# Kernel optimization log

Hardware: AMD Instinct MI355X
Metric: run time of the kernel (lower is better)

The kernel has to match this reference:

```python
import jax, jax.numpy as jnp
import numpy as np
import math

N_HEADS = 16
D_KV = 64
D_MODEL = 1024
NUM_BUCKETS = 32
MAX_DISTANCE = 128


def _relative_position_bucket(rel_pos):
    # encoder (is_decoder=False): bidirectional buckets
    num_buckets = NUM_BUCKETS // 2  # 16
    rel_buckets = (rel_pos > 0).astype(jnp.int32) * num_buckets
    rel_pos = jnp.abs(rel_pos)
    max_exact = num_buckets // 2  # 8
    is_small = rel_pos < max_exact
    rel_pos_large = max_exact + (
        jnp.log(rel_pos.astype(jnp.float32) / max_exact)
        / math.log(MAX_DISTANCE / max_exact)
        * (num_buckets - max_exact)
    ).astype(jnp.int32)
    rel_pos_large = jnp.minimum(rel_pos_large, num_buckets - 1)
    return rel_buckets + jnp.where(is_small, rel_pos, rel_pos_large)


def setup_inputs() -> dict:
    key = jax.random.key(0)
    ks = jax.random.split(key, 6)
    s = 1.0 / math.sqrt(D_MODEL)
    return {
        "hidden_states": jax.random.normal(ks[0], (2, 2048, D_MODEL), jnp.float32),
        "Wq": jax.random.normal(ks[1], (D_MODEL, N_HEADS * D_KV), jnp.float32) * s,
        "Wk": jax.random.normal(ks[2], (D_MODEL, N_HEADS * D_KV), jnp.float32) * s,
        "Wv": jax.random.normal(ks[3], (D_MODEL, N_HEADS * D_KV), jnp.float32) * s,
        "Wo": jax.random.normal(ks[4], (N_HEADS * D_KV, D_MODEL), jnp.float32) * s,
        "rel_bias": jax.random.normal(ks[5], (NUM_BUCKETS, N_HEADS), jnp.float32),
    }


def reference(hidden_states, Wq, Wk, Wv, Wo, rel_bias):
    b, seq, _ = hidden_states.shape
    q = (hidden_states @ Wq).reshape(b, seq, N_HEADS, D_KV)
    k = (hidden_states @ Wk).reshape(b, seq, N_HEADS, D_KV)
    v = (hidden_states @ Wv).reshape(b, seq, N_HEADS, D_KV)

    # relative position bias: [1, n_heads, q_len, k_len]
    ctx = jnp.arange(seq, dtype=jnp.int32)[:, None]
    mem = jnp.arange(seq, dtype=jnp.int32)[None, :]
    buckets = _relative_position_bucket(mem - ctx)  # [q, k]
    pos_bias = rel_bias[buckets]                    # [q, k, h]
    pos_bias = jnp.transpose(pos_bias, (2, 0, 1))[None]  # [1, h, q, k]

    # NOTE: T5-style attention has no 1/sqrt(d) scaling
    attn = jnp.einsum('binc,bjnc->bnij', q, k) + pos_bias
    attn = jax.nn.softmax(attn.astype(jnp.float32), axis=-1).astype(attn.dtype)
    o = jnp.einsum('bnij,bjnc->binc', attn, v).reshape(b, seq, N_HEADS * D_KV)
    return o @ Wo
```

## Files before the change

kernel.cpp:

```cpp
#include <hip/hip_runtime.h>
#include <hip/hip_bf16.h>
#include <math.h>

#define DM   1024
#define HD   1024
#define NH   16
#define DK   64
#define SEQ  2048
#define BATCH 2

#define LOG2E 1.4426950408889634f

typedef __attribute__((ext_vector_type(8))) short bf16x8;
typedef __attribute__((ext_vector_type(4))) float f32x4;

static __device__ __forceinline__ short f2b(float f) {
  union { float f; unsigned u; } v; v.f = f;
  unsigned r = (v.u + 0x7fffu + ((v.u >> 16) & 1u)) >> 16;
  return (short)r;
}

static __device__ __forceinline__ int cvt_pk(float lo, float hi) {
  int r;
  asm("v_cvt_pk_bf16_f32 %0, %1, %2" : "=v"(r) : "v"(lo), "v"(hi));
  return r;
}

static __device__ __forceinline__ void gload_lds16(const void* g, void* l) {
  __builtin_amdgcn_global_load_lds(
      (const __attribute__((address_space(1))) void*)g,
      (__attribute__((address_space(3))) void*)l, 16, 0, 0);
}


__global__ __launch_bounds__(256) void k_cvt_h(const float* __restrict__ in,
                                               short* __restrict__ out) {
  int i = (blockIdx.x * 256 + threadIdx.x) * 8;
  float4 a = *reinterpret_cast<const float4*>(in + i);
  float4 b = *reinterpret_cast<const float4*>(in + i + 4);
  bf16x8 o;
  o[0] = f2b(a.x); o[1] = f2b(a.y); o[2] = f2b(a.z); o[3] = f2b(a.w);
  o[4] = f2b(b.x); o[5] = f2b(b.y); o[6] = f2b(b.z); o[7] = f2b(b.w);
  *reinterpret_cast<bf16x8*>(out + i) = o;
}

__global__ __launch_bounds__(256) void k_wtrans(const float* __restrict__ Wq,
                                                const float* __restrict__ Wk,
                                                const float* __restrict__ Wv,
                                                const float* __restrict__ Wo,
                                                short* __restrict__ Wts) {
  const float* src = (blockIdx.z == 0) ? Wq : (blockIdx.z == 1) ? Wk
                   : (blockIdx.z == 2) ? Wv : Wo;
  const float scl = (blockIdx.z == 0) ? LOG2E : 1.0f;
  short* dst = Wts + (size_t)blockIdx.z * DM * HD;
  __shared__ float t[32][33];
  int tx = threadIdx.x & 31, ty = threadIdx.x >> 5;
  int k0 = blockIdx.y * 32, n0 = blockIdx.x * 32;
#pragma unroll
  for (int i = 0; i < 4; ++i)
    t[ty + i * 8][tx] = src[(size_t)(k0 + ty + i * 8) * 1024 + n0 + tx];
  __syncthreads();
#pragma unroll
  for (int i = 0; i < 4; ++i)
    dst[(size_t)(n0 + ty + i * 8) * 1024 + k0 + tx] = f2b(t[tx][ty + i * 8] * scl);
}

__global__ __launch_bounds__(256) void k_bias(const float* __restrict__ rel_bias,
                                              float* __restrict__ btab) {
  int idx = blockIdx.x * 256 + threadIdx.x;
  int h = idx >> 12, pos = idx & 4095;
  int delta = pos - 2047;
  int rb = (delta > 0) ? 16 : 0;
  int ar = (delta < 0) ? -delta : delta;
  int bb;
  if (ar < 8) bb = ar;
  else {
    bb = 8 + (int)(logf((float)ar * 0.125f) * (8.0f / 2.7725887222397811f));
    if (bb > 15) bb = 15;
  }
  btab[idx] = rel_bias[(rb + bb) * NH + h] * LOG2E;
}

__global__ __launch_bounds__(256) void k_vtrans(const short* __restrict__ Vb,
                                                short* __restrict__ Vt) {
  int bh = blockIdx.y, b = bh >> 4, h = bh & 15;
  int st = blockIdx.x * 64;
  __shared__ short t[64][72];
  int tx = threadIdx.x & 15, ty = threadIdx.x >> 4;
#pragma unroll
  for (int i = 0; i < 4; ++i) {
    int row = ty + i * 16;
    *reinterpret_cast<short4*>(&t[row][tx * 4]) =
        *reinterpret_cast<const short4*>(
            &Vb[(size_t)(b * SEQ + st + row) * HD + h * 64 + tx * 4]);
  }
  __syncthreads();
  const int chunk = tx >> 3, bb = tx & 7;
  const int p = ((bb & 3) << 1) | (bb >> 2);
  const int kvpos = st + chunk * 32 + p * 4;
#pragma unroll
  for (int i = 0; i < 4; ++i) {
    int dk = ty + i * 16;
    short4 v = make_short4(t[tx * 4 + 0][dk], t[tx * 4 + 1][dk],
                           t[tx * 4 + 2][dk], t[tx * 4 + 3][dk]);
    *reinterpret_cast<short4*>(
        &Vt[(size_t)bh * DK * SEQ + (size_t)dk * SEQ + kvpos]) = v;
  }
}

template <int OUTF32>
__global__ __launch_bounds__(256) void k_gemm_bt(const short* __restrict__ A,
                                                 const short* __restrict__ Bt,
                                                 void* __restrict__ Cv,
                                                 size_t btz, size_t cz) {
  __shared__ __align__(16) short As[128 * 32];
  __shared__ __align__(16) short Bs[128 * 32];
  const int tid = threadIdx.x, w = tid >> 6, lane = tid & 63;
  const int wr = w >> 1, wc = w & 1, lg = lane >> 4, l15 = lane & 15;
  const int rowBase = blockIdx.y * 128, colBase = blockIdx.x * 128;
  const short* B = Bt + (size_t)blockIdx.z * btz;

  f32x4 acc[4][4];
#pragma unroll
  for (int m = 0; m < 4; ++m)
#pragma unroll
    for (int n = 0; n < 4; ++n) acc[m][n] = (f32x4){0.f, 0.f, 0.f, 0.f};

  const int c1 = w * 64 + lane, c2 = c1 + 256;
  const short* Ap1 = A + (size_t)(rowBase + (c1 >> 2)) * 1024 + (c1 & 3) * 8;
  const short* Ap2 = A + (size_t)(rowBase + (c2 >> 2)) * 1024 + (c2 & 3) * 8;
  const short* Bp1 = B + (size_t)(colBase + (c1 >> 2)) * 1024 + (c1 & 3) * 8;
  const short* Bp2 = B + (size_t)(colBase + (c2 >> 2)) * 1024 + (c2 & 3) * 8;
  char* AsB = (char*)As;
  char* BsB = (char*)Bs;

  for (int k0 = 0; k0 < 1024; k0 += 32) {
    __syncthreads();
    gload_lds16(Ap1 + k0, AsB + w * 1024);
    gload_lds16(Ap2 + k0, AsB + 4096 + w * 1024);
    gload_lds16(Bp1 + k0, BsB + w * 1024);
    gload_lds16(Bp2 + k0, BsB + 4096 + w * 1024);
    asm volatile("s_waitcnt vmcnt(0)" ::: "memory");
    __syncthreads();
    bf16x8 af[4], bfr[4];
#pragma unroll
    for (int m = 0; m < 4; ++m)
      af[m] = *reinterpret_cast<const bf16x8*>(
          &As[(wr * 64 + m * 16 + l15) * 32 + lg * 8]);
#pragma unroll
    for (int n = 0; n < 4; ++n)
      bfr[n] = *reinterpret_cast<const bf16x8*>(
          &Bs[(wc * 64 + n * 16 + l15) * 32 + lg * 8]);
#pragma unroll
    for (int m = 0; m < 4; ++m)
#pragma unroll
      for (int n = 0; n < 4; ++n)
        acc[m][n] =
            __builtin_amdgcn_mfma_f32_16x16x32_bf16(af[m], bfr[n], acc[m][n], 0, 0, 0);
  }

#pragma unroll
  for (int m = 0; m < 4; ++m)
#pragma unroll
    for (int n = 0; n < 4; ++n) {
      int col = colBase + wc * 64 + n * 16 + l15;
#pragma unroll
      for (int r = 0; r < 4; ++r) {
        int row = rowBase + wr * 64 + m * 16 + lg * 4 + r;
        if (OUTF32)
          ((float*)Cv)[(size_t)row * 1024 + col] = acc[m][n][r];
        else
          ((short*)Cv + (size_t)blockIdx.z * cz)[(size_t)row * 1024 + col] =
              f2b(acc[m][n][r]);
      }
    }
}

static __device__ __forceinline__ void stage_tile(const char* gbase, size_t grs,
                                                  char* lbase, int w, int lane) {
  const int r0 = w * 16 + (lane >> 3);
  const int cb = (lane & 7) * 16;
  const int sw = (r0 & 7) << 4;
  gload_lds16(gbase + (size_t)r0 * grs + (cb ^ sw), lbase + w * 2048);
  gload_lds16(gbase + (size_t)(r0 + 8) * grs + (cb ^ sw), lbase + w * 2048 + 1024);
}

__global__ __launch_bounds__(256, 4) void k_attn(const short* __restrict__ Qb,
                                                 const short* __restrict__ Kb,
                                                 const short* __restrict__ Vt,
                                                 const float* __restrict__ biasTab,
                                                 short* __restrict__ Ob) {
  const int j = blockIdx.x;
  const int orig = (j & 7) * 128 + (j >> 3);
  const int qt = orig & 31, bh = orig >> 5;
  const int b = bh >> 4, h = bh & 15;
  const int w = threadIdx.x >> 6, lane = threadIdx.x & 63;
  const int lg = lane >> 4, l15 = lane & 15;
  const int qbase = qt * 64 + w * 16;

  __shared__ __align__(16) char Ks[2][8192];
  __shared__ __align__(16) char Vs[2][8192];
  const int swz = (l15 & 7) << 4;

  const short* Qrow = Qb + (size_t)(b * SEQ + qbase + l15) * HD + h * 64 + lg * 8;
  bf16x8 q0 = *reinterpret_cast<const bf16x8*>(Qrow);
  bf16x8 q1 = *reinterpret_cast<const bf16x8*>(Qrow + 32);

  const char* Kg = (const char*)(Kb + (size_t)(b * SEQ) * HD + h * 64);
  const char* Vg = (const char*)(Vt + (size_t)bh * DK * SEQ);
  const float* btab = biasTab + h * 4096 + 2047;
  const float bias_hi = btab[1024];
  const float bias_lo = btab[-1024];

  f32x4 o[4];
#pragma unroll
  for (int c = 0; c < 4; ++c) o[c] = (f32x4){0.f, 0.f, 0.f, 0.f};
  float m_r = -INFINITY, l_r = 0.f;

  const f32x4 z4 = (f32x4){0.f, 0.f, 0.f, 0.f};

  stage_tile(Kg, 2048, Ks[0], w, lane);
  stage_tile(Vg, 4096, Vs[0], w, lane);
  asm volatile("s_waitcnt vmcnt(0)" ::: "memory");
  __syncthreads();
  int cur = 0;

  for (int kt = 0; kt < 32; ++kt) {
    const int kvb = kt * 64;
    const int dkv = kvb - qbase;
    if (kt < 31) {
      stage_tile(Kg + (size_t)(kvb + 64) * 2048, 2048, Ks[cur ^ 1], w, lane);
      stage_tile(Vg + (size_t)(kvb + 64) * 2, 4096, Vs[cur ^ 1], w, lane);
    }
    const char* KsC = Ks[cur];
    f32x4 s[4];
    __builtin_amdgcn_s_setprio(1);
#pragma unroll
    for (int c = 0; c < 4; ++c) {
      const char* kr = KsC + (c * 16 + l15) * 128;
      bf16x8 kf0 = *reinterpret_cast<const bf16x8*>(kr + ((lg * 16) ^ swz));
      bf16x8 kf1 = *reinterpret_cast<const bf16x8*>(kr + ((64 + lg * 16) ^ swz));
      s[c] = __builtin_amdgcn_mfma_f32_16x16x32_bf16(kf0, q0, z4, 0, 0, 0);
      s[c] = __builtin_amdgcn_mfma_f32_16x16x32_bf16(kf1, q1, s[c], 0, 0, 0);
    }
    __builtin_amdgcn_s_setprio(0);
    float bu = 0.f;
    if (dkv >= 112) {
      bu = bias_hi;
    } else if (dkv <= -160) {
      bu = bias_lo;
    } else {
#pragma unroll
      for (int c = 0; c < 4; ++c)
#pragma unroll
        for (int r = 0; r < 4; ++r)
          s[c][r] += btab[dkv + c * 16 + lg * 4 + r - l15];
    }
    float u0 = fmaxf(fmaxf(s[0][0], s[0][1]), s[0][2]);
    float u1 = fmaxf(fmaxf(s[0][3], s[1][0]), s[1][1]);
    float u2 = fmaxf(fmaxf(s[1][2], s[1][3]), s[2][0]);
    float u3 = fmaxf(fmaxf(s[2][1], s[2][2]), s[2][3]);
    float u4 = fmaxf(fmaxf(s[3][0], s[3][1]), s[3][2]);
    float v0 = fmaxf(fmaxf(u0, u1), u2);
    float v1 = fmaxf(fmaxf(u3, u4), s[3][3]);
    float mx = fmaxf(v0, v1);
    mx = fmaxf(mx, __shfl_xor(mx, 16, 64));
    mx = fmaxf(mx, __shfl_xor(mx, 32, 64));
    mx += bu;
    if (!__all(mx <= m_r + 8.0f)) {
      float mn = fmaxf(m_r, mx);
      float sc = __builtin_exp2f(m_r - mn);
      m_r = mn;
      l_r *= sc;
#pragma unroll
      for (int c = 0; c < 4; ++c)
#pragma unroll
        for (int r = 0; r < 4; ++r) o[c][r] *= sc;
    }
    const float mb = m_r - bu;
#pragma unroll
    for (int c = 0; c < 4; ++c)
#pragma unroll
      for (int r = 0; r < 4; ++r) s[c][r] = __builtin_exp2f(s[c][r] - mb);
    float r0 = (s[0][0] + s[0][1]) + (s[0][2] + s[0][3]);
    float r1 = (s[1][0] + s[1][1]) + (s[1][2] + s[1][3]);
    float r2 = (s[2][0] + s[2][1]) + (s[2][2] + s[2][3]);
    float r3 = (s[3][0] + s[3][1]) + (s[3][2] + s[3][3]);
    float rs = (r0 + r1) + (r2 + r3);
    rs += __shfl_xor(rs, 16, 64);
    rs += __shfl_xor(rs, 32, 64);
    l_r += rs;
    int4 p0i, p1i;
    p0i.x = cvt_pk(s[0][0], s[0][1]); p0i.y = cvt_pk(s[0][2], s[0][3]);
    p0i.z = cvt_pk(s[1][0], s[1][1]); p0i.w = cvt_pk(s[1][2], s[1][3]);
    p1i.x = cvt_pk(s[2][0], s[2][1]); p1i.y = cvt_pk(s[2][2], s[2][3]);
    p1i.z = cvt_pk(s[3][0], s[3][1]); p1i.w = cvt_pk(s[3][2], s[3][3]);
    bf16x8 pb0 = *reinterpret_cast<bf16x8*>(&p0i);
    bf16x8 pb1 = *reinterpret_cast<bf16x8*>(&p1i);
    const char* VsC = Vs[cur];
    __builtin_amdgcn_s_setprio(1);
#pragma unroll
    for (int d = 0; d < 4; ++d) {
      const char* vr = VsC + (d * 16 + l15) * 128;
      bf16x8 v0f = *reinterpret_cast<const bf16x8*>(vr + ((lg * 16) ^ swz));
      bf16x8 v1f = *reinterpret_cast<const bf16x8*>(vr + ((64 + lg * 16) ^ swz));
      o[d] = __builtin_amdgcn_mfma_f32_16x16x32_bf16(v0f, pb0, o[d], 0, 0, 0);
      o[d] = __builtin_amdgcn_mfma_f32_16x16x32_bf16(v1f, pb1, o[d], 0, 0, 0);
    }
    __builtin_amdgcn_s_setprio(0);
    asm volatile("s_waitcnt vmcnt(0)" ::: "memory");
    __syncthreads();
    cur ^= 1;
  }
  float inv = 1.0f / l_r;
  const size_t orow = (size_t)(b * SEQ + qbase + l15) * HD + h * 64;
#pragma unroll
  for (int d = 0; d < 4; ++d) {
    int2 e;
    e.x = cvt_pk(o[d][0] * inv, o[d][1] * inv);
    e.y = cvt_pk(o[d][2] * inv, o[d][3] * inv);
    *reinterpret_cast<int2*>(&Ob[orow + d * 16 + lg * 4]) = e;
  }
}

extern "C" void kernel_launch(void* const* d_in, const int* in_sizes, int n_in,
                              void* d_out, int out_size, void* d_ws, size_t ws_size,
                              hipStream_t stream) {
  const float* H    = (const float*)d_in[0];
  const float* Wq   = (const float*)d_in[1];
  const float* Wk   = (const float*)d_in[2];
  const float* Wv   = (const float*)d_in[3];
  const float* Wo   = (const float*)d_in[4];
  const float* relb = (const float*)d_in[5];

  char* ws = (char*)d_ws;
  short* Hb   = (short*)(ws);
  short* Wts  = (short*)(ws + ((size_t)8 << 20));
  short* Qb   = (short*)(ws + ((size_t)16 << 20));
  short* Kb   = (short*)(ws + ((size_t)24 << 20));
  short* Vb   = (short*)(ws + ((size_t)32 << 20));
  short* Vt   = (short*)(ws + ((size_t)40 << 20));
  short* Ob   = (short*)(ws + ((size_t)48 << 20));
  float* btab = (float*)(ws + ((size_t)56 << 20));

  k_cvt_h<<<2048, 256, 0, stream>>>(H, Hb);
  k_wtrans<<<dim3(32, 32, 4), 256, 0, stream>>>(Wq, Wk, Wv, Wo, Wts);
  k_bias<<<256, 256, 0, stream>>>(relb, btab);

  k_gemm_bt<0><<<dim3(8, 32, 3), 256, 0, stream>>>(
      Hb, Wts, Qb, (size_t)1024 * 1024, (size_t)4096 * 1024);

  k_vtrans<<<dim3(32, 32), 256, 0, stream>>>(Vb, Vt);
  k_attn<<<1024, 256, 0, stream>>>(Qb, Kb, Vt, btab, Ob);

  k_gemm_bt<1><<<dim3(8, 32, 1), 256, 0, stream>>>(
      Ob, Wts + (size_t)3 * 1024 * 1024, d_out, 0, 0);
}
```

Measured before the change: 221.0 us.

## Double-buffer GEMM LDS tiles and defer attention row-sum reduction to end

The projection GEMM now keeps two LDS buffers for A and B. It prefetches the next K-slice while the MFMAs consume the current one, leaving one barrier per iteration instead of two. In the attention kernel, the cross-lane shuffle reduction of the softmax row sum moves out of the KV loop and runs once after it. This is valid because every lane's partial sum is rescaled by the same per-row max factor. The cost is double the LDS use in the GEMM, which may lower occupancy.

```diff
diff --git a/kernel.cpp b/kernel.cpp
--- a/kernel.cpp
+++ b/kernel.cpp
@@ -113,8 +113,8 @@
                                                  const short* __restrict__ Bt,
                                                  void* __restrict__ Cv,
                                                  size_t btz, size_t cz) {
-  __shared__ __align__(16) short As[128 * 32];
-  __shared__ __align__(16) short Bs[128 * 32];
+  __shared__ __align__(16) short As[2][128 * 32];
+  __shared__ __align__(16) short Bs[2][128 * 32];
   const int tid = threadIdx.x, w = tid >> 6, lane = tid & 63;
   const int wr = w >> 1, wc = w & 1, lg = lane >> 4, l15 = lane & 15;
   const int rowBase = blockIdx.y * 128, colBase = blockIdx.x * 128;
@@ -131,32 +131,46 @@
   const short* Ap2 = A + (size_t)(rowBase + (c2 >> 2)) * 1024 + (c2 & 3) * 8;
   const short* Bp1 = B + (size_t)(colBase + (c1 >> 2)) * 1024 + (c1 & 3) * 8;
   const short* Bp2 = B + (size_t)(colBase + (c2 >> 2)) * 1024 + (c2 & 3) * 8;
-  char* AsB = (char*)As;
-  char* BsB = (char*)Bs;
+
+  {
+    char* AsB = (char*)As[0];
+    char* BsB = (char*)Bs[0];
+    gload_lds16(Ap1, AsB + w * 1024);
+    gload_lds16(Ap2, AsB + 4096 + w * 1024);
+    gload_lds16(Bp1, BsB + w * 1024);
+    gload_lds16(Bp2, BsB + 4096 + w * 1024);
+  }
+  asm volatile("s_waitcnt vmcnt(0)" ::: "memory");
+  __syncthreads();
+  int cur = 0;
 
   for (int k0 = 0; k0 < 1024; k0 += 32) {
-    __syncthreads();
-    gload_lds16(Ap1 + k0, AsB + w * 1024);
-    gload_lds16(Ap2 + k0, AsB + 4096 + w * 1024);
-    gload_lds16(Bp1 + k0, BsB + w * 1024);
-    gload_lds16(Bp2 + k0, BsB + 4096 + w * 1024);
-    asm volatile("s_waitcnt vmcnt(0)" ::: "memory");
-    __syncthreads();
+    if (k0 + 32 < 1024) {
+      char* AsB = (char*)As[cur ^ 1];
+      char* BsB = (char*)Bs[cur ^ 1];
+      gload_lds16(Ap1 + k0 + 32, AsB + w * 1024);
+      gload_lds16(Ap2 + k0 + 32, AsB + 4096 + w * 1024);
+      gload_lds16(Bp1 + k0 + 32, BsB + w * 1024);
+      gload_lds16(Bp2 + k0 + 32, BsB + 4096 + w * 1024);
+    }
     bf16x8 af[4], bfr[4];
 #pragma unroll
     for (int m = 0; m < 4; ++m)
       af[m] = *reinterpret_cast<const bf16x8*>(
-          &As[(wr * 64 + m * 16 + l15) * 32 + lg * 8]);
+          &As[cur][(wr * 64 + m * 16 + l15) * 32 + lg * 8]);
 #pragma unroll
     for (int n = 0; n < 4; ++n)
       bfr[n] = *reinterpret_cast<const bf16x8*>(
-          &Bs[(wc * 64 + n * 16 + l15) * 32 + lg * 8]);
+          &Bs[cur][(wc * 64 + n * 16 + l15) * 32 + lg * 8]);
 #pragma unroll
     for (int m = 0; m < 4; ++m)
 #pragma unroll
       for (int n = 0; n < 4; ++n)
         acc[m][n] =
             __builtin_amdgcn_mfma_f32_16x16x32_bf16(af[m], bfr[n], acc[m][n], 0, 0, 0);
+    asm volatile("s_waitcnt vmcnt(0)" ::: "memory");
+    __syncthreads();
+    cur ^= 1;
   }
 
 #pragma unroll
@@ -286,10 +300,7 @@
     float r1 = (s[1][0] + s[1][1]) + (s[1][2] + s[1][3]);
     float r2 = (s[2][0] + s[2][1]) + (s[2][2] + s[2][3]);
     float r3 = (s[3][0] + s[3][1]) + (s[3][2] + s[3][3]);
-    float rs = (r0 + r1) + (r2 + r3);
-    rs += __shfl_xor(rs, 16, 64);
-    rs += __shfl_xor(rs, 32, 64);
-    l_r += rs;
+    l_r += (r0 + r1) + (r2 + r3);
     int4 p0i, p1i;
     p0i.x = cvt_pk(s[0][0], s[0][1]); p0i.y = cvt_pk(s[0][2], s[0][3]);
     p0i.z = cvt_pk(s[1][0], s[1][1]); p0i.w = cvt_pk(s[1][2], s[1][3]);
@@ -312,6 +323,8 @@
     __syncthreads();
     cur ^= 1;
   }
+  l_r += __shfl_xor(l_r, 16, 64);
+  l_r += __shfl_xor(l_r, 32, 64);
   float inv = 1.0f / l_r;
   const size_t orow = (size_t)(b * SEQ + qbase + l15) * HD + h * 64;
 #pragma unroll
```

Result: no change. 222.9 us (+0.9%).
